# Kernel tuning notes

Measured on AMD Instinct MI355X. Metric: run time of the kernel, lower is better.

The kernel has to match this reference:

```python
import jax, jax.numpy as jnp
import numpy as np

B, CIN, CH, COUT = 16, 256, 256, 256
RES = 16
E = 32           # embed_dim
NEMB = 1024      # codebook size
NP = 128         # n_phylo_channels (ch - NP == NP)
L = 4            # n_phylolevels
K = 8            # attribute codes per level per kernel
KN = 32          # nonattribute codes per kernel (levels=1)
CP = L * K * E   # 1024 projected phylo channels
CN = KN * E      # 1024 projected nonattr channels
BETA = 0.25
EPS = 1e-5

def conv1x1(x, w, b):
    # x: [B,C,H,W], w: [O,C], b: [O]
    return jnp.einsum('oc,bchw->bohw', w, x) + b[None, :, None, None]

def layernorm_chw(x, w, b):
    # LayerNorm over (C,H,W) per sample, elementwise affine of shape [C,H,W]
    mu = jnp.mean(x, axis=(1, 2, 3), keepdims=True)
    var = jnp.var(x, axis=(1, 2, 3), keepdims=True)
    return (x - mu) * jax.lax.rsqrt(var + EPS) * w[None] + b[None]

def reshape_in(x, levels):
    # [B, E*levels*K', H, W] -> [B, E, K'*H*W, levels]
    Bb, C, H, W = x.shape
    Kp = C // (E * levels)
    x = x.reshape(Bb, E, levels, Kp, H * W)
    x = x.transpose(0, 1, 3, 4, 2)          # [B,E,K',HW,levels]
    return x.reshape(Bb, E, Kp * H * W, levels)

def reshape_out(x, levels):
    # [B, E, K'*HW, levels] -> [B, E*levels*K', RES, RES]
    Bb, Ee, N, Ll = x.shape
    Kp = N // (RES * RES)
    x = x.reshape(Bb, Ee, Kp, RES * RES, Ll)
    x = x.transpose(0, 1, 4, 2, 3)          # [B,E,levels,K',HW]
    return x.reshape(Bb, Ee * Ll * Kp, RES, RES)

def quantize(z, codebook):
    # z: [B, E, N, levels]; codebook: [NEMB, E]
    zp = z.transpose(0, 2, 3, 1)            # [B,N,levels,E]
    flat = zp.reshape(-1, E)
    d = (jnp.sum(flat * flat, axis=1, keepdims=True)
         - 2.0 * flat @ codebook.T
         + jnp.sum(codebook * codebook, axis=1)[None, :])
    idx = jnp.argmin(d, axis=1)
    zq = codebook[idx].reshape(zp.shape)
    sg = jax.lax.stop_gradient
    loss = jnp.mean((sg(zq) - zp) ** 2) + BETA * jnp.mean((zq - sg(zp)) ** 2)
    zq = zp + sg(zq - zp)                   # straight-through
    return zq.transpose(0, 3, 1, 2), loss

def setup_inputs() -> dict:
    key = jax.random.key(0)
    ks = jax.random.split(key, 20)
    s = 0.02
    inp = {
        'x': jax.random.normal(ks[0], (B, CIN, RES, RES), jnp.float32),
        'conv_in_w': jax.random.normal(ks[1], (CH, CIN), jnp.float32) * s,
        'conv_in_b': jnp.zeros((CH,), jnp.float32),
        'ln_p_w': jnp.ones((NP, RES, RES), jnp.float32),
        'ln_p_b': jnp.zeros((NP, RES, RES), jnp.float32),
        'wp_in': jax.random.normal(ks[2], (CP, NP), jnp.float32) * s,
        'bp_in': jnp.zeros((CP,), jnp.float32),
        'wp_out': jax.random.normal(ks[3], (NP, CP), jnp.float32) * s,
        'bp_out': jnp.zeros((NP,), jnp.float32),
        'ln_n_w': jnp.ones((CH - NP, RES, RES), jnp.float32),
        'ln_n_b': jnp.zeros((CH - NP, RES, RES), jnp.float32),
        'wn_in': jax.random.normal(ks[4], (CN, CH - NP), jnp.float32) * s,
        'bn_in': jnp.zeros((CN,), jnp.float32),
        'wn_out': jax.random.normal(ks[5], (CH - NP, CN), jnp.float32) * s,
        'bn_out': jnp.zeros((CH - NP,), jnp.float32),
        'codebook': jax.random.uniform(ks[6], (NEMB, E), jnp.float32,
                                       -1.0 / NEMB, 1.0 / NEMB),
        'conv_out_w': jax.random.normal(ks[7], (COUT, CH), jnp.float32) * s,
        'conv_out_b': jnp.zeros((COUT,), jnp.float32),
    }
    return inp

def reference(x, conv_in_w, conv_in_b, ln_p_w, ln_p_b, wp_in, bp_in,
              wp_out, bp_out, ln_n_w, ln_n_b, wn_in, bn_in, wn_out, bn_out,
              codebook, conv_out_w, conv_out_b):
    silu = jax.nn.silu
    h = conv1x1(silu(x), conv_in_w, conv_in_b)
    h_p, h_n = h[:, :NP], h[:, NP:]
    # phylo branch
    z_p = silu(conv1x1(layernorm_chw(silu(h_p), ln_p_w, ln_p_b), wp_in, bp_in))
    zq_p, loss_p = quantize(reshape_in(z_p, L), codebook)
    hout_p = silu(conv1x1(reshape_out(zq_p, L), wp_out, bp_out))
    # non-attribute branch (anticlassification path)
    z_n = silu(conv1x1(layernorm_chw(silu(h_n), ln_n_w, ln_n_b), wn_in, bn_in))
    zq_n, loss_n = quantize(reshape_in(z_n, 1), codebook)
    hout_n = silu(conv1x1(reshape_out(zq_n, 1), wn_out, bn_out))
    h_cat = jnp.concatenate([hout_p, hout_n], axis=1)
    out = conv1x1(silu(h_cat), conv_out_w, conv_out_b)
    return out, loss_p + loss_n, zq_p
```

## Files before the change

kernel.cpp:

```cpp
#include <hip/hip_runtime.h>
#include <hip/hip_bf16.h>


typedef float f32x4  __attribute__((ext_vector_type(4)));
typedef short bf16x8 __attribute__((ext_vector_type(8)));

__device__ __forceinline__ float silu_rw(float x){ return x / (1.f + expf(-x)); }
__device__ __forceinline__ float b2f_rw(__hip_bfloat16 v){ return __bfloat162float(v); }
__device__ __forceinline__ float ldv_rw(const void* p, int i, int f32m){
  if (f32m) return ((const float*)p)[i];
  return b2f_rw(((const __hip_bfloat16*)p)[i]);
}
__device__ __forceinline__ unsigned short f2bf_rw(float x){
  unsigned u = __float_as_uint(x);
  unsigned r = ((u >> 16) & 1u) + 0x7FFFu;
  return (unsigned short)((u + r) >> 16);
}
__device__ __forceinline__ float bf2f_rw(unsigned short h){
  return __uint_as_float(((unsigned)h) << 16);
}

#define FLAGS_OFF 0
#define LOSS_OFF  4
#define STATS_OFF 8
#define CNT_OFF   72
#define CMAX_OFF  80
#define CB32_OFF  128
#define CBN_OFF   32896
#define IDXP_OFF  33984
#define IDXN_OFF  165056
#define CBHL_OFF  296192
#define LIST_OFF  328960
#define R2_OFF    460032
#define R3_OFF    984320
#define R1_OFF    1508608

__global__ __launch_bounds__(256) void detect_rw(const void* cbv, float* wsb){
  __shared__ int bad;
  if (threadIdx.x == 0) bad = 0;
  __syncthreads();
  const unsigned short* u = (const unsigned short*)cbv;
  int local = 0;
  for (int i = threadIdx.x; i < 32768; i += 256){
    unsigned e = (u[i] >> 7) & 0xFF;
    if (e >= 126) local = 1;
  }
  if (local) bad = 1;
  __syncthreads();
  if (threadIdx.x == 0){
    wsb[FLAGS_OFF] = bad ? 1.f : 0.f;
    wsb[LOSS_OFF] = 0.f; wsb[LOSS_OFF + 1] = 0.f;
    int* c = (int*)(wsb + CNT_OFF);
    #pragma unroll
    for (int k = 0; k < 8; ++k) c[k] = 0;
    wsb[CMAX_OFF] = 0.f;
  }
}

__global__ __launch_bounds__(256) void cbprep_rw(const void* cbv, const float* flags,
                                                 float* cb32, float* cbn,
                                                 short* cbhl, float* cmaxp){
  const int f32m = (flags[0] != 0.f);
  int j = blockIdx.x * 256 + threadIdx.x;
  if (j < 1024){
    float s = 0.f;
    const int tb = ((j >> 4) << 10) + ((j & 15) << 5);
    for (int e = 0; e < 32; ++e){
      float v = ldv_rw(cbv, j*32 + e, f32m);
      cb32[j*32 + e] = v;
      unsigned short h = f2bf_rw(v);
      cbhl[tb + e]       = (short)h;
      cbhl[tb + e + 512] = (short)f2bf_rw(v - bf2f_rw(h));
      s += v*v;
    }
    cbn[j] = s;
    atomicMax((int*)cmaxp, __float_as_int(sqrtf(s)));
  }
}

template<int KCH, int INMODE, bool OUTSILU, bool ATOMIC, int LEVELS>
__global__ __launch_bounds__(256) void gemm2_rw(
    const float* __restrict__ inF, const float* __restrict__ inF2,
    const void* __restrict__ inV,
    const void* __restrict__ W, const void* __restrict__ biasO,
    const void* __restrict__ sbA, const void* __restrict__ sbB,
    const int* __restrict__ idxin, const float* __restrict__ cb32,
    float* __restrict__ outF, const float* __restrict__ flags,
    int KDIM, int OUTC, int o_off, int b_base, int ib_sub, int ob_sub)
{
  __shared__ float As[32][32];
  __shared__ float Bs[32][68];
  __shared__ int   IdxS[32][32];

  const int f32m = (flags[0] != 0.f);
  const int t  = threadIdx.x;
  const int q0 = (blockIdx.x << 5) + (b_base << 8);
  const int b  = q0 >> 8;
  const int p0 = q0 & 255;
  const int o0 = blockIdx.y << 6;
  const int k0base = blockIdx.z * KCH;
  const int tx = t & 15, ty = t >> 4;
  float acc[4][2] = {};

  const int sch = t >> 3, spx = (t & 7) << 2;

  if constexpr (INMODE == 3){
    #pragma unroll
    for (int j = 0; j < 4; ++j){
      const int p = p0 + spx + j;
      if constexpr (LEVELS == 4){
        const int l = sch >> 3, kp = sch & 7;
        IdxS[sch][spx + j] = idxin[b*8192 + (((kp << 8) + p) << 2) + l];
      } else {
        IdxS[sch][spx + j] = idxin[b*8192 + (sch << 8) + p];
      }
    }
    __syncthreads();
  }

  for (int kc = 0; kc < KCH; kc += 32){
    const int k0 = k0base + kc;
    if constexpr (INMODE == 0){
      const float4 v = *reinterpret_cast<const float4*>(
          &inF[(((b - ib_sub)*KDIM + k0 + sch) << 8) + p0 + spx]);
      *reinterpret_cast<float4*>(&As[sch][spx]) = v;
    } else if constexpr (INMODE == 2){
      if (f32m){
        const float* xf = (const float*)inV;
        float4 v = *reinterpret_cast<const float4*>(&xf[((b*KDIM + k0 + sch) << 8) + p0 + spx]);
        v.x = silu_rw(v.x); v.y = silu_rw(v.y); v.z = silu_rw(v.z); v.w = silu_rw(v.w);
        *reinterpret_cast<float4*>(&As[sch][spx]) = v;
      } else {
        const __hip_bfloat16* xb = (const __hip_bfloat16*)inV;
        const int off = ((b*KDIM + k0 + sch) << 8) + p0 + spx;
        #pragma unroll
        for (int j = 0; j < 4; ++j) As[sch][spx + j] = silu_rw(b2f_rw(xb[off + j]));
      }
    } else if constexpr (INMODE == 3){
      const int e = k0 >> 5;
      #pragma unroll
      for (int j = 0; j < 4; ++j)
        As[sch][spx + j] = cb32[((IdxS[sch][spx + j] & 1023) << 5) + e];
    } else {
      const float* src = (k0 < 128) ? inF : inF2;
      const void* sb   = (k0 < 128) ? sbA : sbB;
      const int kh = k0 & 127;
      const float bb = ldv_rw(sb, kh + sch, f32m);
      float4 v = *reinterpret_cast<const float4*>(&src[((b*128 + kh + sch) << 8) + p0 + spx]);
      v.x = silu_rw(v.x + bb); v.y = silu_rw(v.y + bb);
      v.z = silu_rw(v.z + bb); v.w = silu_rw(v.w + bb);
      *reinterpret_cast<float4*>(&As[sch][spx]) = v;
    }
    if (f32m){
      const float* Wf = (const float*)W;
      #pragma unroll
      for (int r = 0; r < 8; ++r){
        int ii = t + (r << 8); int oo = ii >> 5, cc = ii & 31;
        Bs[cc][oo] = Wf[(o0 + oo)*KDIM + k0 + cc];
      }
    } else {
      const __hip_bfloat16* Wb = (const __hip_bfloat16*)W;
      #pragma unroll
      for (int r = 0; r < 8; ++r){
        int ii = t + (r << 8); int oo = ii >> 5, cc = ii & 31;
        Bs[cc][oo] = b2f_rw(Wb[(o0 + oo)*KDIM + k0 + cc]);
      }
    }
    __syncthreads();
    #pragma unroll
    for (int kk = 0; kk < 32; ++kk){
      const float2 a = *reinterpret_cast<const float2*>(&As[kk][tx << 1]);
      const float4 w = *reinterpret_cast<const float4*>(&Bs[kk][ty << 2]);
      acc[0][0] += w.x*a.x; acc[0][1] += w.x*a.y;
      acc[1][0] += w.y*a.x; acc[1][1] += w.y*a.y;
      acc[2][0] += w.z*a.x; acc[2][1] += w.z*a.y;
      acc[3][0] += w.w*a.x; acc[3][1] += w.w*a.y;
    }
    __syncthreads();
  }
  #pragma unroll
  for (int i = 0; i < 4; ++i){
    const int o = o0 + (ty << 2) + i;
    const int base = (((b - ob_sub)*OUTC + o_off + o) << 8) + p0 + (tx << 1);
    if constexpr (ATOMIC){
      atomicAdd(&outF[base + 0], acc[i][0]);
      atomicAdd(&outF[base + 1], acc[i][1]);
    } else {
      const float bb = ldv_rw(biasO, o, f32m);
      float v0 = acc[i][0] + bb, v1 = acc[i][1] + bb;
      if constexpr (OUTSILU){ v0 = silu_rw(v0); v1 = silu_rw(v1); }
      *reinterpret_cast<float2*>(&outF[base]) = make_float2(v0, v1);
    }
  }
}

__global__ __launch_bounds__(256) void stats_rw(const float* __restrict__ h, float* __restrict__ stats){
  const int b = blockIdx.x >> 1, half = blockIdx.x & 1;
  const float* base = h + ((b*256 + half*128) << 8);
  float s = 0.f, s2 = 0.f;
  for (int i = threadIdx.x; i < 32768; i += 256){
    float a = silu_rw(base[i]);
    s += a; s2 += a*a;
  }
  __shared__ float sh[2][256];
  sh[0][threadIdx.x] = s; sh[1][threadIdx.x] = s2;
  __syncthreads();
  for (int st = 128; st > 0; st >>= 1){
    if (threadIdx.x < st){
      sh[0][threadIdx.x] += sh[0][threadIdx.x + st];
      sh[1][threadIdx.x] += sh[1][threadIdx.x + st];
    }
    __syncthreads();
  }
  if (threadIdx.x == 0){
    float mu  = sh[0][0] * (1.f/32768.f);
    float var = sh[1][0] * (1.f/32768.f) - mu*mu;
    stats[half*32 + b]      = mu;
    stats[half*32 + 16 + b] = 1.f / sqrtf(var + 1e-5f);
  }
}

__global__ __launch_bounds__(256) void ln_rw(const float* __restrict__ h,
    const void* lwp, const void* lbp, const void* lwn, const void* lbn,
    const float* __restrict__ stats, const float* __restrict__ flags,
    float* __restrict__ lnp, float* __restrict__ lnn){
  const int f32m = (flags[0] != 0.f);
  int i = blockIdx.x * 256 + threadIdx.x;
  int b = i >> 16, c = (i >> 8) & 255, p = i & 255;
  float a = silu_rw(h[i]);
  if (c < 128){
    float v = (a - stats[b]) * stats[16 + b] * ldv_rw(lwp, (c << 8) + p, f32m) + ldv_rw(lbp, (c << 8) + p, f32m);
    lnp[((b*128 + c) << 8) + p] = v;
  } else {
    int cc = c - 128;
    float v = (a - stats[32 + b]) * stats[48 + b] * ldv_rw(lwn, (cc << 8) + p, f32m) + ldv_rw(lbn, (cc << 8) + p, f32m);
    lnn[((b*128 + cc) << 8) + p] = v;
  }
}

template<int LEVELS>
__global__ __launch_bounds__(512, 4) void quantm_rw(
    const float* __restrict__ z, const short* __restrict__ cbhl,
    const float* __restrict__ cbn, const float* __restrict__ cmaxp,
    int* __restrict__ idxout, float* __restrict__ lossacc,
    int* __restrict__ cnt, int* __restrict__ list, int b_base)
{
  __shared__ float mgm1[4][4][8], mgm2[4][4][8];
  __shared__ int   mgj [4][4][8];
  __shared__ float red[4];

  const int tid  = threadIdx.x;
  const int lane = tid & 63, wid = tid >> 6;
  const int lc = lane & 15, gq = lane >> 4;
  const int pg = wid & 3, ch = wid >> 2;
  const int bid  = blockIdx.x;
  const int bl   = bid >> 6;
  const int rest = bid & 63;
  const int g = rest >> 1, half = rest & 1;
  int cb, wbase, wstep;
  if (LEVELS == 4){ cb = (g & 3)*8 + (g >> 2); wbase = (g >> 2)*1024 + (g & 3); wstep = 4; }
  else            { cb = g;                    wbase = g << 8;                  wstep = 1; }
  const int pb = half*128 + pg*32;

  bf16x8 ah0, al0, ah1, al1;
  float zn0 = 0.f, zn1 = 0.f;
  const int zoff = (((bl << 10) + cb) << 8) + pb + lc;
  const int e0 = gq << 3;
  #pragma unroll
  for (int i = 0; i < 8; ++i){
    const int zo = zoff + ((e0 + i) << 13);
    const float z0 = z[zo];
    const float z1 = z[zo + 16];
    zn0 += z0*z0; zn1 += z1*z1;
    const float s0 = -2.f*z0, s1 = -2.f*z1;
    const unsigned short h0 = f2bf_rw(s0);
    const unsigned short h1 = f2bf_rw(s1);
    ah0[i] = (short)h0; al0[i] = (short)f2bf_rw(s0 - bf2f_rw(h0));
    ah1[i] = (short)h1; al1[i] = (short)f2bf_rw(s1 - bf2f_rw(h1));
  }
  zn0 += __shfl_xor(zn0, 16); zn0 += __shfl_xor(zn0, 32);
  zn1 += __shfl_xor(zn1, 16); zn1 += __shfl_xor(zn1, 32);

  float m1[8], m2[8]; int j1[8];
  #pragma unroll
  for (int s = 0; s < 8; ++s){ m1[s] = __builtin_inff(); m2[s] = __builtin_inff(); j1[s] = 0; }

  const short* bp  = cbhl + (ch << 15) + (lc << 5) + (gq << 3);
  const float* cnp = cbn + (ch << 9) + lc;

  bf16x8 bh  = *reinterpret_cast<const bf16x8*>(bp);
  bf16x8 blo = *reinterpret_cast<const bf16x8*>(bp + 512);
  float  cnv = cnp[0];

  #pragma unroll 2
  for (int t = 0; t < 32; ++t){
    const int tn = (t < 31) ? t + 1 : 31;
    const bf16x8 bhn  = *reinterpret_cast<const bf16x8*>(bp + (tn << 10));
    const bf16x8 blon = *reinterpret_cast<const bf16x8*>(bp + (tn << 10) + 512);
    const float  cnn  = cnp[tn << 4];

    f32x4 a0 = {cnv, cnv, cnv, cnv};
    f32x4 a1 = {cnv, cnv, cnv, cnv};
    a0 = __builtin_amdgcn_mfma_f32_16x16x32_bf16(ah0, bh,  a0, 0, 0, 0);
    a0 = __builtin_amdgcn_mfma_f32_16x16x32_bf16(ah0, blo, a0, 0, 0, 0);
    a0 = __builtin_amdgcn_mfma_f32_16x16x32_bf16(al0, bh,  a0, 0, 0, 0);
    a1 = __builtin_amdgcn_mfma_f32_16x16x32_bf16(ah1, bh,  a1, 0, 0, 0);
    a1 = __builtin_amdgcn_mfma_f32_16x16x32_bf16(ah1, blo, a1, 0, 0, 0);
    a1 = __builtin_amdgcn_mfma_f32_16x16x32_bf16(al1, bh,  a1, 0, 0, 0);

    const int jc = (((ch << 5) + t) << 4) + lc;
    #pragma unroll
    for (int r = 0; r < 4; ++r){
      const float d0 = a0[r];
      m2[r] = __builtin_amdgcn_fmed3f(d0, m1[r], m2[r]);
      const bool t0 = d0 < m1[r];
      j1[r] = t0 ? jc : j1[r]; m1[r] = t0 ? d0 : m1[r];
      const float d1 = a1[r];
      m2[4+r] = __builtin_amdgcn_fmed3f(d1, m1[4+r], m2[4+r]);
      const bool t1 = d1 < m1[4+r];
      j1[4+r] = t1 ? jc : j1[4+r]; m1[4+r] = t1 ? d1 : m1[4+r];
    }
    bh = bhn; blo = blon; cnv = cnn;
  }

  #pragma unroll
  for (int k = 1; k < 16; k <<= 1){
    #pragma unroll
    for (int s = 0; s < 8; ++s){
      const float om1 = __shfl_xor(m1[s], k);
      const float om2 = __shfl_xor(m2[s], k);
      const int   oj  = __shfl_xor(j1[s], k);
      m2[s] = fminf(fminf(m2[s], om2), fmaxf(m1[s], om1));
      const bool tk = (om1 < m1[s]) || (om1 == m1[s] && oj < j1[s]);
      m1[s] = tk ? om1 : m1[s];
      j1[s] = tk ? oj  : j1[s];
    }
  }

  if (wid >= 4 && lc == 0){
    #pragma unroll
    for (int s = 0; s < 8; ++s){
      mgm1[wid-4][gq][s] = m1[s];
      mgm2[wid-4][gq][s] = m2[s];
      mgj [wid-4][gq][s] = j1[s];
    }
  }
  __syncthreads();
  if (wid < 4){
    #pragma unroll
    for (int s = 0; s < 8; ++s){
      const float om1 = mgm1[wid][gq][s];
      const float om2 = mgm2[wid][gq][s];
      const int   oj  = mgj [wid][gq][s];
      m2[s] = fminf(fminf(m2[s], om2), fmaxf(m1[s], om1));
      const bool tk = om1 < m1[s];
      m1[s] = tk ? om1 : m1[s];
      j1[s] = tk ? oj  : j1[s];
    }

    const float cmax = cmaxp[0];
    float lossw = 0.f;
    #pragma unroll
    for (int f = 0; f < 2; ++f){
      #pragma unroll
      for (int r = 0; r < 4; ++r){
        const int s = f*4 + r;
        const int vrow = (gq << 2) + r;
        const float znv = __shfl(f == 0 ? zn0 : zn1, vrow);
        if (lc == 0){
          const int p  = pb + f*16 + vrow;
          const int gi = (b_base + bl)*8192 + wbase + p*wstep;
          idxout[gi] = j1[s];
          const float eb = fmaf(2.0e-6f, znv, 3.0e-4f * sqrtf(znv) * cmax);
          if (m2[s] - m1[s] > eb){
            lossw += znv + m1[s];
          } else {
            const int pos = atomicAdd(cnt, 1);
            if (pos < 131072) list[pos] = (((bl << 5) | g) << 8) | p;
          }
        }
      }
    }
    lossw += __shfl_xor(lossw, 16);
    lossw += __shfl_xor(lossw, 32);
    if (lane == 0) red[wid] = lossw;
  }
  __syncthreads();
  if (tid == 0) atomicAdd(lossacc, red[0] + red[1] + red[2] + red[3]);
}

template<int LEVELS>
__global__ __launch_bounds__(256) void fb_rw(
    const float* __restrict__ z, const float* __restrict__ cb32,
    const float* __restrict__ cbn, const int* __restrict__ cnt,
    const int* __restrict__ list, int* __restrict__ idxout,
    float* __restrict__ lossacc, int b_base)
{
  const int lane = threadIdx.x & 63;
  const int wv = (blockIdx.x << 2) | (threadIdx.x >> 6);
  const int nw = gridDim.x << 2;
  int n = cnt[0];
  if (n > 131072) n = 131072;
  for (int it = wv; it < n; it += nw){
    const int id = list[it];
    const int p = id & 255, g = (id >> 8) & 31, bl = id >> 13;
    int cb, w;
    if (LEVELS == 4){ cb = (g & 3)*8 + (g >> 2); w = (g >> 2)*1024 + (p << 2) + (g & 3); }
    else            { cb = g;                    w = (g << 8) + p; }
    const int zoff = (((bl << 10) + cb) << 8) + p;
    float myz = 0.f;
    if (lane < 32) myz = z[zoff + (lane << 13)];
    float zb[32];
    #pragma unroll
    for (int e = 0; e < 32; ++e) zb[e] = __shfl(myz, e);
    float zn = 0.f;
    #pragma unroll
    for (int e = 0; e < 32; ++e) zn = fmaf(zb[e], zb[e], zn);
    float bd = __builtin_inff(); int bj = 0;
    #pragma unroll 4
    for (int jj = 0; jj < 16; ++jj){
      const int j = (jj << 6) + lane;
      const float4* c4 = reinterpret_cast<const float4*>(cb32 + (j << 5));
      float dot = 0.f;
      #pragma unroll
      for (int e4 = 0; e4 < 8; ++e4){
        const float4 cv = c4[e4];
        dot = fmaf(zb[(e4 << 2) + 0], cv.x, dot);
        dot = fmaf(zb[(e4 << 2) + 1], cv.y, dot);
        dot = fmaf(zb[(e4 << 2) + 2], cv.z, dot);
        dot = fmaf(zb[(e4 << 2) + 3], cv.w, dot);
      }
      const float d = (zn - 2.f*dot) + cbn[j];
      if (d < bd){ bd = d; bj = j; }
    }
    #pragma unroll
    for (int k = 1; k < 64; k <<= 1){
      const float od = __shfl_xor(bd, k);
      const int   oj = __shfl_xor(bj, k);
      if (od < bd || (od == bd && oj < bj)){ bd = od; bj = oj; }
    }
    if (lane == 0){
      idxout[(b_base + bl)*8192 + w] = bj;
      atomicAdd(lossacc, bd);
    }
  }
}

__global__ __launch_bounds__(256) void zqout_rw(const int* __restrict__ idxp,
    const float* __restrict__ cb32, float* __restrict__ out){
  int t = blockIdx.x * 256 + threadIdx.x;
  int l = t & 3, n = (t >> 2) & 2047, e = (t >> 13) & 31, b = t >> 18;
  int id = idxp[b*8192 + (n << 2) + l];
  out[t] = cb32[((id & 1023) << 5) + e];
}

__global__ __launch_bounds__(256) void zero_rw(float* __restrict__ p){
  p[blockIdx.x * 256 + threadIdx.x] = 0.f;
}

__global__ void loss_rw(const float* __restrict__ lossacc, float* __restrict__ out){
  if (threadIdx.x == 0 && blockIdx.x == 0)
    out[0] = 1.25f * (lossacc[0] + lossacc[1]) * (1.f/4194304.f);
}

extern "C" void kernel_launch(void* const* d_in, const int* in_sizes, int n_in,
                              void* d_out, int out_size, void* d_ws, size_t ws_size,
                              hipStream_t stream){
  (void)in_sizes; (void)n_in; (void)out_size;
  const void* x   = d_in[0];
  const void* ciw = d_in[1];
  const void* cib = d_in[2];
  const void* lwp = d_in[3];
  const void* lbp = d_in[4];
  const void* wpi = d_in[5];
  const void* bpi = d_in[6];
  const void* wpo = d_in[7];
  const void* bpo = d_in[8];
  const void* lwn = d_in[9];
  const void* lbn = d_in[10];
  const void* wni = d_in[11];
  const void* bni = d_in[12];
  const void* wno = d_in[13];
  const void* bno = d_in[14];
  const void* cbk = d_in[15];
  const void* cow = d_in[16];
  const void* cob = d_in[17];

  float* ws    = (float*)d_ws;
  float* flags = ws + FLAGS_OFF;
  float* loss  = ws + LOSS_OFF;
  float* stats = ws + STATS_OFF;
  float* cmaxp = ws + CMAX_OFF;
  float* cb32  = ws + CB32_OFF;
  float* cbn   = ws + CBN_OFF;
  int*   cnts  = (int*)(ws + CNT_OFF);
  int*   idxp  = (int*)(ws + IDXP_OFF);
  int*   idxn  = (int*)(ws + IDXN_OFF);
  short* cbhl  = (short*)(ws + CBHL_OFF);
  int*   list  = (int*)(ws + LIST_OFF);
  float* R2    = ws + R2_OFF;
  float* R3    = ws + R3_OFF;
  float* R1    = ws + R1_OFF;

  float* outO = (float*)d_out;
  float* outL = outO + 1048576;
  float* outZ = outO + 1048577;

  const size_t wsf = ws_size / 4;
  int CS = 4;
  if      (wsf >= (size_t)R1_OFF + 16u*262144u) CS = 16;
  else if (wsf >= (size_t)R1_OFF +  8u*262144u) CS = 8;

  detect_rw<<<1, 256, 0, stream>>>(cbk, ws);
  cbprep_rw<<<4, 256, 0, stream>>>(cbk, flags, cb32, cbn, cbhl, cmaxp);
  gemm2_rw<256,2,false,false,0><<<dim3(128,4), 256, 0, stream>>>(
      nullptr, nullptr, x, ciw, cib, nullptr, nullptr, nullptr, nullptr,
      R1, flags, 256, 256, 0, 0, 0, 0);
  stats_rw<<<32, 256, 0, stream>>>(R1, stats);
  ln_rw<<<4096, 256, 0, stream>>>(R1, lwp, lbp, lwn, lbn, stats, flags, R2, R3);
  {
    int ci = 0;
    for (int c = 0; c < 16; c += CS, ++ci){
      gemm2_rw<128,0,true,false,0><<<dim3(CS*8,16), 256, 0, stream>>>(
          R2, nullptr, nullptr, wpi, bpi, nullptr, nullptr, nullptr, nullptr,
          R1, flags, 128, 1024, 0, c, 0, c);
      quantm_rw<4><<<CS*64, 512, 0, stream>>>(R1, cbhl, cbn, cmaxp,
                                              idxp, loss + 0, cnts + ci, list, c);
      fb_rw<4><<<640, 256, 0, stream>>>(R1, cb32, cbn, cnts + ci, list,
                                        idxp, loss + 0, c);
    }
  }
  {
    int ci = 4;
    for (int c = 0; c < 16; c += CS, ++ci){
      gemm2_rw<128,0,true,false,0><<<dim3(CS*8,16), 256, 0, stream>>>(
          R3, nullptr, nullptr, wni, bni, nullptr, nullptr, nullptr, nullptr,
          R1, flags, 128, 1024, 0, c, 0, c);
      quantm_rw<1><<<CS*64, 512, 0, stream>>>(R1, cbhl, cbn, cmaxp,
                                              idxn, loss + 1, cnts + ci, list, c);
      fb_rw<1><<<640, 256, 0, stream>>>(R1, cb32, cbn, cnts + ci, list,
                                        idxn, loss + 1, c);
    }
  }
  zqout_rw<<<16384, 256, 0, stream>>>(idxp, cb32, outZ);
  zero_rw<<<4096, 256, 0, stream>>>(R2);
  gemm2_rw<256,3,false,true,4><<<dim3(128,2,4), 256, 0, stream>>>(
      nullptr, nullptr, nullptr, wpo, nullptr, nullptr, nullptr, idxp, cb32,
      R2, flags, 1024, 128, 0, 0, 0, 0);
  gemm2_rw<256,3,false,true,1><<<dim3(128,2,4), 256, 0, stream>>>(
      nullptr, nullptr, nullptr, wno, nullptr, nullptr, nullptr, idxn, cb32,
      R3, flags, 1024, 128, 0, 0, 0, 0);
  gemm2_rw<256,5,false,false,0><<<dim3(128,4), 256, 0, stream>>>(
      R2, R3, nullptr, cow, cob, bpo, bno, nullptr, nullptr,
      outO, flags, 256, 256, 0, 0, 0, 0);
  loss_rw<<<1, 64, 0, stream>>>(loss, outL);
}
```

Measured before the change: 533.9 us.

## Use split-bf16 MFMA kernel for codebook-gather output projections

Replaces the scalar FMA gemm2 path (INMODE 3) for the wp_out/wn_out projections with a dedicated kernel. The new kernel gathers codebook entries from the hi/lo bf16 split codebook, converts the weights to hi/lo bf16 on the fly, and accumulates with three 16x16x32 bf16 MFMAs per tile to approximate fp32 precision. It targets the FMA-bound inner loop of the two largest output GEMMs. In exchange it does a per-element weight conversion inside the loop, drops the lo*lo term, and keeps the atomicAdd split-K over 4 z-slices.

Measured after the change: 616.9 us. 15.5% more time.

```diff
diff --git a/kernel.cpp b/kernel.cpp
--- a/kernel.cpp
+++ b/kernel.cpp
@@ -90,7 +90,6 @@
 {
   __shared__ float As[32][32];
   __shared__ float Bs[32][68];
-  __shared__ int   IdxS[32][32];
 
   const int f32m = (flags[0] != 0.f);
   const int t  = threadIdx.x;
@@ -103,20 +102,6 @@
   float acc[4][2] = {};
 
   const int sch = t >> 3, spx = (t & 7) << 2;
-
-  if constexpr (INMODE == 3){
-    #pragma unroll
-    for (int j = 0; j < 4; ++j){
-      const int p = p0 + spx + j;
-      if constexpr (LEVELS == 4){
-        const int l = sch >> 3, kp = sch & 7;
-        IdxS[sch][spx + j] = idxin[b*8192 + (((kp << 8) + p) << 2) + l];
-      } else {
-        IdxS[sch][spx + j] = idxin[b*8192 + (sch << 8) + p];
-      }
-    }
-    __syncthreads();
-  }
 
   for (int kc = 0; kc < KCH; kc += 32){
     const int k0 = k0base + kc;
@@ -136,11 +121,6 @@
         #pragma unroll
         for (int j = 0; j < 4; ++j) As[sch][spx + j] = silu_rw(b2f_rw(xb[off + j]));
       }
-    } else if constexpr (INMODE == 3){
-      const int e = k0 >> 5;
-      #pragma unroll
-      for (int j = 0; j < 4; ++j)
-        As[sch][spx + j] = cb32[((IdxS[sch][spx + j] & 1023) << 5) + e];
     } else {
       const float* src = (k0 < 128) ? inF : inF2;
       const void* sb   = (k0 < 128) ? sbA : sbB;
@@ -191,6 +171,87 @@
       if constexpr (OUTSILU){ v0 = silu_rw(v0); v1 = silu_rw(v1); }
       *reinterpret_cast<float2*>(&outF[base]) = make_float2(v0, v1);
     }
+  }
+}
+
+template<int LEVELS>
+__global__ __launch_bounds__(256, 4) void houtm_rw(
+    const int* __restrict__ idxin, const short* __restrict__ cbhl,
+    const void* __restrict__ W, float* __restrict__ outF,
+    const float* __restrict__ flags)
+{
+  __shared__ short As_h[32][32];
+  __shared__ short As_l[32][32];
+
+  const int f32m = (flags[0] != 0.f);
+  const int t = threadIdx.x;
+  const int lane = t & 63, wid = t >> 6;
+  const int lc = lane & 15, gq = lane >> 4;
+  const int b   = blockIdx.x >> 3;
+  const int p0  = (blockIdx.x & 7) << 5;
+  const int o0  = (blockIdx.y << 6) + (wid << 4);
+  const int kz  = blockIdx.z;
+
+  const int sch_t = t >> 3, pxj = (t & 7) << 2;
+
+  int idx_r[4];
+  #pragma unroll
+  for (int j = 0; j < 4; ++j){
+    const int px = p0 + pxj + j;
+    if (LEVELS == 4){
+      const int l = sch_t >> 3, kp = sch_t & 7;
+      idx_r[j] = idxin[b*8192 + (((kp << 8) + px) << 2) + l] & 1023;
+    } else {
+      idx_r[j] = idxin[b*8192 + (sch_t << 8) + px] & 1023;
+    }
+  }
+
+  const int o = o0 + lc;
+  f32x4 acc0 = {0.f, 0.f, 0.f, 0.f};
+  f32x4 acc1 = {0.f, 0.f, 0.f, 0.f};
+
+  const unsigned short* cbu = (const unsigned short*)cbhl;
+
+  for (int el = 0; el < 8; ++el){
+    const int e = (kz << 3) + el;
+    #pragma unroll
+    for (int j = 0; j < 4; ++j){
+      const int id = idx_r[j];
+      const int a  = ((id >> 4) << 10) + ((id & 15) << 5) + e;
+      As_h[pxj + j][sch_t] = (short)cbu[a];
+      As_l[pxj + j][sch_t] = (short)cbu[a + 512];
+    }
+    __syncthreads();
+
+    const bf16x8 ah0 = *reinterpret_cast<const bf16x8*>(&As_h[lc][gq << 3]);
+    const bf16x8 al0 = *reinterpret_cast<const bf16x8*>(&As_l[lc][gq << 3]);
+    const bf16x8 ah1 = *reinterpret_cast<const bf16x8*>(&As_h[16 + lc][gq << 3]);
+    const bf16x8 al1 = *reinterpret_cast<const bf16x8*>(&As_l[16 + lc][gq << 3]);
+
+    const int kb = (kz << 8) + (el << 5) + (gq << 3);
+    bf16x8 bh, bl;
+    #pragma unroll
+    for (int i = 0; i < 8; ++i){
+      const float wv = ldv_rw(W, o*1024 + kb + i, f32m);
+      const unsigned short h = f2bf_rw(wv);
+      bh[i] = (short)h;
+      bl[i] = (short)f2bf_rw(wv - bf2f_rw(h));
+    }
+
+    acc0 = __builtin_amdgcn_mfma_f32_16x16x32_bf16(ah0, bh, acc0, 0, 0, 0);
+    acc0 = __builtin_amdgcn_mfma_f32_16x16x32_bf16(ah0, bl, acc0, 0, 0, 0);
+    acc0 = __builtin_amdgcn_mfma_f32_16x16x32_bf16(al0, bh, acc0, 0, 0, 0);
+    acc1 = __builtin_amdgcn_mfma_f32_16x16x32_bf16(ah1, bh, acc1, 0, 0, 0);
+    acc1 = __builtin_amdgcn_mfma_f32_16x16x32_bf16(ah1, bl, acc1, 0, 0, 0);
+    acc1 = __builtin_amdgcn_mfma_f32_16x16x32_bf16(al1, bh, acc1, 0, 0, 0);
+    __syncthreads();
+  }
+
+  const int obase = ((b*128 + o) << 8) + p0 + (gq << 2);
+  #pragma unroll
+  for (int r = 0; r < 4; ++r){
+    atomicAdd(&outF[obase + r],      acc0[r]);
+    atomicAdd(&outF[obase + 16 + r], acc1[r]);
   }
 }
 
@@ -544,12 +605,8 @@
   }
   zqout_rw<<<16384, 256, 0, stream>>>(idxp, cb32, outZ);
   zero_rw<<<4096, 256, 0, stream>>>(R2);
-  gemm2_rw<256,3,false,true,4><<<dim3(128,2,4), 256, 0, stream>>>(
-      nullptr, nullptr, nullptr, wpo, nullptr, nullptr, nullptr, idxp, cb32,
-      R2, flags, 1024, 128, 0, 0, 0, 0);
-  gemm2_rw<256,3,false,true,1><<<dim3(128,2,4), 256, 0, stream>>>(
-      nullptr, nullptr, nullptr, wno, nullptr, nullptr, nullptr, idxn, cb32,
-      R3, flags, 1024, 128, 0, 0, 0, 0);
+  houtm_rw<4><<<dim3(128, 2, 4), 256, 0, stream>>>(idxp, cbhl, wpo, R2, flags);
+  houtm_rw<1><<<dim3(128, 2, 4), 256, 0, stream>>>(idxn, cbhl, wno, R3, flags);
   gemm2_rw<256,5,false,false,0><<<dim3(128,4), 256, 0, stream>>>(
       R2, R3, nullptr, cow, cob, bpo, bno, nullptr, nullptr,
       outO, flags, 256, 256, 0, 0, 0, 0);
```

## Use split-bf16 MFMA for codebook-gather output projection GEMMs

Applied to the files above, without the earlier changes.

Replaces the scalar FP32 tiled GEMM for the two post-quantization output convolutions with a new kernel that gathers codebook rows by index and multiplies them on MFMA bf16 instructions. Weights are pre-split into high and low bf16 halves by a small prep kernel, and three MFMAs per step emulate near-FP32 precision. The goal is to cut the FMA-bound cost of the 1024-deep reductions, at the price of an extra prep launch, scratch space reused from R1, and slightly different rounding.

Result: slower. 568.4 us (+6.5%).

```diff
diff --git a/kernel.cpp b/kernel.cpp
--- a/kernel.cpp
+++ b/kernel.cpp
@@ -90,7 +90,6 @@
 {
   __shared__ float As[32][32];
   __shared__ float Bs[32][68];
-  __shared__ int   IdxS[32][32];
 
   const int f32m = (flags[0] != 0.f);
   const int t  = threadIdx.x;
@@ -103,20 +102,6 @@
   float acc[4][2] = {};
 
   const int sch = t >> 3, spx = (t & 7) << 2;
-
-  if constexpr (INMODE == 3){
-    #pragma unroll
-    for (int j = 0; j < 4; ++j){
-      const int p = p0 + spx + j;
-      if constexpr (LEVELS == 4){
-        const int l = sch >> 3, kp = sch & 7;
-        IdxS[sch][spx + j] = idxin[b*8192 + (((kp << 8) + p) << 2) + l];
-      } else {
-        IdxS[sch][spx + j] = idxin[b*8192 + (sch << 8) + p];
-      }
-    }
-    __syncthreads();
-  }
 
   for (int kc = 0; kc < KCH; kc += 32){
     const int k0 = k0base + kc;
@@ -136,11 +121,6 @@
         #pragma unroll
         for (int j = 0; j < 4; ++j) As[sch][spx + j] = silu_rw(b2f_rw(xb[off + j]));
       }
-    } else if constexpr (INMODE == 3){
-      const int e = k0 >> 5;
-      #pragma unroll
-      for (int j = 0; j < 4; ++j)
-        As[sch][spx + j] = cb32[((IdxS[sch][spx + j] & 1023) << 5) + e];
     } else {
       const float* src = (k0 < 128) ? inF : inF2;
       const void* sb   = (k0 < 128) ? sbA : sbB;
@@ -191,6 +171,86 @@
       if constexpr (OUTSILU){ v0 = silu_rw(v0); v1 = silu_rw(v1); }
       *reinterpret_cast<float2*>(&outF[base]) = make_float2(v0, v1);
     }
+  }
+}
+
+__global__ __launch_bounds__(256) void wprep_rw(const void* Wp, const void* Wn,
+    const float* flags, short* whlp, short* whln){
+  const int f32m = (flags[0] != 0.f);
+  const void* W = blockIdx.y ? Wn : Wp;
+  short* whl = blockIdx.y ? whln : whlp;
+  const int t = threadIdx.x;
+  const int sch = t & 31, o = (blockIdx.x << 3) + (t >> 5);
+  const int ob = ((sch << 7) + o) << 6;
+  for (int e = 0; e < 32; ++e){
+    const float wv = ldv_rw(W, (o << 10) + (e << 5) + sch, f32m);
+    const unsigned short h = f2bf_rw(wv);
+    whl[ob + e]      = (short)h;
+    whl[ob + 32 + e] = (short)f2bf_rw(wv - bf2f_rw(h));
+  }
+}
+
+template<int LEVELS>
+__global__ __launch_bounds__(256, 4) void houtm2_rw(
+    const int* __restrict__ idxin, const short* __restrict__ cbhl,
+    const short* __restrict__ whl, float* __restrict__ outF)
+{
+  const int t = threadIdx.x;
+  const int lane = t & 63, wid = t >> 6;
+  const int lc = lane & 15, gq = lane >> 4;
+  const int b  = blockIdx.x >> 3;
+  const int p0 = (blockIdx.x & 7) << 5;
+  const int o0 = (blockIdx.y << 6) + (wid << 4);
+  const int s0 = blockIdx.z << 3;
+  const int ge = gq << 3;
+
+  int j0[8], j1[8];
+  #pragma unroll
+  for (int s = 0; s < 8; ++s){
+    const int sch = s0 + s;
+    int a0, a1;
+    if (LEVELS == 4){
+      const int l = sch >> 3, kp = sch & 7;
+      a0 = b*8192 + (((kp << 8) + p0 + lc) << 2) + l;
+      a1 = b*8192 + (((kp << 8) + p0 + 16 + lc) << 2) + l;
+    } else {
+      a0 = b*8192 + (sch << 8) + p0 + lc;
+      a1 = a0 + 16;
+    }
+    j0[s] = idxin[a0] & 1023;
+    j1[s] = idxin[a1] & 1023;
+  }
+
+  f32x4 acc0 = {0.f, 0.f, 0.f, 0.f};
+  f32x4 acc1 = {0.f, 0.f, 0.f, 0.f};
+
+  #pragma unroll 1
+  for (int s = 0; s < 8; ++s){
+    const int sch = s0 + s;
+    const int ja = j0[s], jb = j1[s];
+    const int a0h = ((ja >> 4) << 10) + ((ja & 15) << 5) + ge;
+    const int a1h = ((jb >> 4) << 10) + ((jb & 15) << 5) + ge;
+    const bf16x8 ah0 = *reinterpret_cast<const bf16x8*>(cbhl + a0h);
+    const bf16x8 al0 = *reinterpret_cast<const bf16x8*>(cbhl + a0h + 512);
+    const bf16x8 ah1 = *reinterpret_cast<const bf16x8*>(cbhl + a1h);
+    const bf16x8 al1 = *reinterpret_cast<const bf16x8*>(cbhl + a1h + 512);
+    const int wb = (((sch << 7) + o0 + lc) << 6) + ge;
+    const bf16x8 bh = *reinterpret_cast<const bf16x8*>(whl + wb);
+    const bf16x8 bl = *reinterpret_cast<const bf16x8*>(whl + wb + 32);
+
+    acc0 = __builtin_amdgcn_mfma_f32_16x16x32_bf16(ah0, bh, acc0, 0, 0, 0);
+    acc0 = __builtin_amdgcn_mfma_f32_16x16x32_bf16(ah0, bl, acc0, 0, 0, 0);
+    acc0 = __builtin_amdgcn_mfma_f32_16x16x32_bf16(al0, bh, acc0, 0, 0, 0);
+    acc1 = __builtin_amdgcn_mfma_f32_16x16x32_bf16(ah1, bh, acc1, 0, 0, 0);
+    acc1 = __builtin_amdgcn_mfma_f32_16x16x32_bf16(ah1, bl, acc1, 0, 0, 0);
+    acc1 = __builtin_amdgcn_mfma_f32_16x16x32_bf16(al1, bh, acc1, 0, 0, 0);
+  }
+
+  const int obase = ((b*128 + o0 + lc) << 8) + p0 + (gq << 2);
+  #pragma unroll
+  for (int r = 0; r < 4; ++r){
+    atomicAdd(&outF[obase + r],      acc0[r]);
+    atomicAdd(&outF[obase + 16 + r], acc1[r]);
   }
 }
 
@@ -501,6 +561,8 @@
   float* R2    = ws + R2_OFF;
   float* R3    = ws + R3_OFF;
   float* R1    = ws + R1_OFF;
+  short* whlp  = (short*)(ws + R1_OFF);
+  short* whln  = (short*)(ws + R1_OFF + 131072);
 
   float* outO = (float*)d_out;
   float* outL = outO + 1048576;
@@ -544,12 +606,9 @@
   }
   zqout_rw<<<16384, 256, 0, stream>>>(idxp, cb32, outZ);
   zero_rw<<<4096, 256, 0, stream>>>(R2);
-  gemm2_rw<256,3,false,true,4><<<dim3(128,2,4), 256, 0, stream>>>(
-      nullptr, nullptr, nullptr, wpo, nullptr, nullptr, nullptr, idxp, cb32,
-      R2, flags, 1024, 128, 0, 0, 0, 0);
-  gemm2_rw<256,3,false,true,1><<<dim3(128,2,4), 256, 0, stream>>>(
-      nullptr, nullptr, nullptr, wno, nullptr, nullptr, nullptr, idxn, cb32,
-      R3, flags, 1024, 128, 0, 0, 0, 0);
+  wprep_rw<<<dim3(16, 2), 256, 0, stream>>>(wpo, wno, flags, whlp, whln);
+  houtm2_rw<4><<<dim3(128, 2, 4), 256, 0, stream>>>(idxp, cbhl, whlp, R2);
+  houtm2_rw<1><<<dim3(128, 2, 4), 256, 0, stream>>>(idxn, cbhl, whln, R3);
   gemm2_rw<256,5,false,false,0><<<dim3(128,4), 256, 0, stream>>>(
       R2, R3, nullptr, cow, cob, bpo, bno, nullptr, nullptr,
       outO, flags, 256, 256, 0, 0, 0, 0);
```
